# Performance work log

Hardware: AMD Instinct MI355X
Metric: run time of the kernel (lower is better)

Reference implementation:

```python
import jax, jax.numpy as jnp
import numpy as np

B, H, D, DV, N, M = 1, 8, 64, 64, 2048, 128


def setup_inputs() -> dict:
    key = jax.random.key(0)
    k1, k2, k3, k4 = jax.random.split(key, 4)
    keys = jax.random.normal(k1, (B, H, D, N), dtype=jnp.float32)
    values = jax.random.normal(k2, (B, H, DV, N), dtype=jnp.float32)
    queries = jax.random.normal(k3, (B, H, D, N), dtype=jnp.float32)
    # orthonormal random features: QR of (m, key_dim) gaussian (reduced QR, m >= key_dim)
    raw = np.asarray(jax.random.normal(k4, (M, D), dtype=jnp.float32), dtype=np.float64)
    features = jnp.asarray(np.linalg.qr(raw)[0], dtype=jnp.float32)  # (M, D)
    return {"keys": keys, "values": values, "queries": queries, "features": features}


def reference(keys, values, queries, features):
    b, h, d, n = keys.shape
    dv = values.shape[2]
    m = features.shape[0]
    phi_scale = 1.0 / jnp.sqrt(jnp.asarray(m, keys.dtype))
    # flatten heads into batch, move locations to axis 1: (B*H, N, D)
    k = keys.reshape(b * h, d, n).transpose(0, 2, 1)
    v = values.reshape(b * h, dv, n).transpose(0, 2, 1)
    q = queries.reshape(b * h, d, n).transpose(0, 2, 1)

    def phi(x):  # (BH, N, D) -> (BH, N, M); f=[relu], h(x)=1.0
        return jax.nn.relu(jnp.einsum('bnd,md->bnm', x, features)) * phi_scale

    phi_k = phi(k)
    phi_q = phi(q)
    # causal linear attention: prefix sums of phi_k (x) v outer products
    kv = jnp.cumsum(phi_k[:, :, :, None] * v[:, :, None, :], axis=1)  # (BH, N, M, DV)
    out = jnp.einsum('bnm,bnmv->bnv', phi_q, kv)                      # (BH, N, DV)
    norm = jnp.einsum('bnm,bnm->bn', phi_q, jnp.cumsum(phi_k, axis=1))
    out = out / norm[:, :, None]
    out = out.transpose(0, 2, 1).reshape(b, h, dv, n)
    return out
```

## Files before the change

kernel.cpp:

```cpp
#include <hip/hip_runtime.h>


#define BH 8
#define DD 64
#define DV 64
#define NSEQ 2048
#define MM 128
#define CK 32
#define NCH 64
#define NBLK 256
#define PHI_SCALE 0.08838834764831845f

typedef unsigned int uint;
typedef unsigned short ushort;
typedef unsigned long long ulong64;
typedef __attribute__((ext_vector_type(8))) short bf16x8;
typedef __attribute__((ext_vector_type(4))) float f32x4;
#define MFMA16(a, b, c) __builtin_amdgcn_mfma_f32_16x16x32_bf16((a), (b), (c), 0, 0, 0)

__device__ __forceinline__ short f2bf(float x) {
    uint u = __float_as_uint(x);
    u += 0x7fffu + ((u >> 16) & 1u);
    return (short)(u >> 16);
}
__device__ __forceinline__ float bf2f(ushort b) {
    return __uint_as_float(((uint)b) << 16);
}

#define AST(p, v)  __hip_atomic_store((p), (v), __ATOMIC_RELAXED, __HIP_MEMORY_SCOPE_AGENT)
#define ALD(p)     __hip_atomic_load((p), __ATOMIC_RELAXED, __HIP_MEMORY_SCOPE_AGENT)

#define OFF_Z   8388608u
#define OFF_BAR 8650752u

__device__ __forceinline__ void gbar(uint* cnt)
{
    __syncthreads();
    if (threadIdx.x == 0) {
        __hip_atomic_fetch_add(cnt, 1u, __ATOMIC_RELAXED, __HIP_MEMORY_SCOPE_AGENT);
        while (__hip_atomic_load(cnt, __ATOMIC_RELAXED, __HIP_MEMORY_SCOPE_AGENT) < NBLK)
            __builtin_amdgcn_s_sleep(4);
    }
    __syncthreads();
}

__global__ __launch_bounds__(256, 2) void favor_main(
    const float* __restrict__ keys, const float* __restrict__ values,
    const float* __restrict__ queries, const float* __restrict__ features,
    ushort* St, float* z, uint* bar, float* __restrict__ out)
{
    const int b = blockIdx.x;
    const int bh = b >> 5, pr_ = b & 31;
    const int tid = threadIdx.x;
    const int lane = tid & 63, wid = tid >> 6, quad = lane >> 4, l16 = lane & 15;
    const int ch = wid >> 1, sw = wid & 1;
    const int ck = 2 * pr_ + ch, n0c = ck * CK;

    __shared__ __align__(16) char sm[60672];
    short* sPQT = (short*)sm;
    short* sPKT = (short*)(sm + 17408);
    short* sPK  = (short*)(sm + 34816);
    short* sAm  = (short*)(sm + 55296);
    float* sNI  = (float*)(sm + 60416);
    float* sOut = (float*)(sm + 17408);
    float* sPart= (float*)(sm + 34816);
    float* sNm  = (float*)(sm + 36352);
    float* sZ   = (float*)(sm + 36608);

    short* pqt = sPQT + ch * 4352;
    short* pkt = sPKT + ch * 4352;
    short* ppk = sPK + ch * 5120;

    for (int i = tid; i < 1280; i += 256) ((uint*)sAm)[i] = 0u;

    {
        const float* Qb = queries + (size_t)(bh * DD) * NSEQ + n0c + 16 * sw + l16;
        const float* Kb = keys    + (size_t)(bh * DD) * NSEQ + n0c + 16 * sw + l16;
        bf16x8 aQ[2], aK[2];
        for (int h = 0; h < 2; ++h)
            for (int j = 0; j < 8; ++j) {
                const int d = 32 * h + 8 * quad + j;
                aQ[h][j] = f2bf(Qb[(size_t)d * NSEQ]);
                aK[h][j] = f2bf(Kb[(size_t)d * NSEQ]);
            }
        for (int mt = 0; mt < 8; ++mt) {
            f32x4 accQ = {0.f, 0.f, 0.f, 0.f}, accK = {0.f, 0.f, 0.f, 0.f};
            for (int h = 0; h < 2; ++h) {
                const float4* fp = (const float4*)(features + (16 * mt + l16) * 64 + 32 * h + 8 * quad);
                float4 f0 = fp[0], f1 = fp[1];
                bf16x8 bF;
                bF[0] = f2bf(f0.x); bF[1] = f2bf(f0.y); bF[2] = f2bf(f0.z); bF[3] = f2bf(f0.w);
                bF[4] = f2bf(f1.x); bF[5] = f2bf(f1.y); bF[6] = f2bf(f1.z); bF[7] = f2bf(f1.w);
                accQ = MFMA16(aQ[h], bF, accQ);
                accK = MFMA16(aK[h], bF, accK);
            }
            for (int r = 0; r < 4; ++r) {
                const int nl = 16 * sw + 4 * quad + r, m = 16 * mt + l16;
                pqt[nl * 136 + m] = f2bf(fmaxf(accQ[r], 0.f) * PHI_SCALE);
                const short pk = f2bf(fmaxf(accK[r], 0.f) * PHI_SCALE);
                pkt[nl * 136 + m] = pk;
                ppk[m * 40 + nl] = pk;
            }
        }
    }
    __syncthreads();

    {
        const int zch = tid >> 7, m = tid & 127;
        const short* pp = sPK + zch * 5120 + m * 40;
        float s = 0.f;
        for (int n = 0; n < CK; ++n) s += bf2f((ushort)pp[(n + m) & 31]);
        AST(&z[(size_t)(bh * NCH + 2 * pr_ + zch) * MM + m], s);
    }

    {
        ushort* So = St + (size_t)(bh * NCH + ck) * (DV * MM);
        const float* Vb = values + (size_t)(bh * DV) * NSEQ + n0c;
        for (int t = 0; t < 2; ++t) {
            const int vt = 2 * sw + t;
            const float4* vp = (const float4*)(Vb + (size_t)(16 * vt + l16) * NSEQ + 8 * quad);
            float4 v0 = vp[0], v1 = vp[1];
            bf16x8 aV;
            aV[0] = f2bf(v0.x); aV[1] = f2bf(v0.y); aV[2] = f2bf(v0.z); aV[3] = f2bf(v0.w);
            aV[4] = f2bf(v1.x); aV[5] = f2bf(v1.y); aV[6] = f2bf(v1.z); aV[7] = f2bf(v1.w);
            for (int mt = 0; mt < 8; ++mt) {
                bf16x8 bP = *(const bf16x8*)(ppk + (16 * mt + l16) * 40 + 8 * quad);
                f32x4 acc = {0.f, 0.f, 0.f, 0.f};
                acc = MFMA16(aV, bP, acc);
                for (int r = 0; r < 4; ++r)
                    AST(&So[(16 * vt + 4 * quad + r) * MM + 16 * mt + l16],
                        (ushort)f2bf(acc[r]));
            }
        }
    }

    {
        float rs[4] = {0.f, 0.f, 0.f, 0.f};
        for (int jt = 0; jt <= sw; ++jt) {
            f32x4 acc = {0.f, 0.f, 0.f, 0.f};
            for (int mc = 0; mc < 4; ++mc) {
                bf16x8 aP = *(const bf16x8*)(pqt + (16 * sw + l16) * 136 + 32 * mc + 8 * quad);
                bf16x8 bP = *(const bf16x8*)(pkt + (16 * jt + l16) * 136 + 32 * mc + 8 * quad);
                acc = MFMA16(aP, bP, acc);
            }
            for (int r = 0; r < 4; ++r) {
                const int nl = 16 * sw + 4 * quad + r, jl = 16 * jt + l16;
                const float av = (jl <= nl) ? acc[r] : 0.f;
                rs[r] += av;
                sAm[ch * 1280 + nl * 40 + jl] = f2bf(av);
            }
        }
        for (int r = 0; r < 4; ++r) {
            float s = rs[r];
            s += __shfl_xor(s, 1); s += __shfl_xor(s, 2);
            s += __shfl_xor(s, 4); s += __shfl_xor(s, 8);
            if (l16 == 0) sNI[ch * 32 + 16 * sw + 4 * quad + r] = s;
        }
    }

    f32x4 acc[4];
    {
        bf16x8 aA = *(const bf16x8*)(sAm + ch * 1280 + (16 * sw + l16) * 40 + 8 * quad);
        const float* Vb = values + (size_t)(bh * DV) * NSEQ + n0c;
        for (int vt = 0; vt < 4; ++vt) {
            const float4* vp = (const float4*)(Vb + (size_t)(16 * vt + l16) * NSEQ + 8 * quad);
            float4 v0 = vp[0], v1 = vp[1];
            bf16x8 bV;
            bV[0] = f2bf(v0.x); bV[1] = f2bf(v0.y); bV[2] = f2bf(v0.z); bV[3] = f2bf(v0.w);
            bV[4] = f2bf(v1.x); bV[5] = f2bf(v1.y); bV[6] = f2bf(v1.z); bV[7] = f2bf(v1.w);
            acc[vt] = (f32x4){0.f, 0.f, 0.f, 0.f};
            acc[vt] = MFMA16(aA, bV, acc[vt]);
        }
    }

    gbar(bar + 0);
    if (b < 128) {
        const int gid = b * 256 + tid;
        const int sbh = gid >> 12, col = gid & 4095;
        uint* p = (uint*)St + (size_t)sbh * (NCH * 4096) + col;
        float rlo = 0.f, rhi = 0.f;
        for (int half = 0; half < 2; ++half) {
            uint v[32];
            #pragma unroll
            for (int cc = 0; cc < 32; ++cc)
                v[cc] = ALD(p + (size_t)(32 * half + cc) * 4096);
            #pragma unroll
            for (int cc = 0; cc < 32; ++cc) {
                const uint ov = (uint)(ushort)f2bf(rlo) | ((uint)(ushort)f2bf(rhi) << 16);
                AST(p + (size_t)(32 * half + cc) * 4096, ov);
                rlo += bf2f((ushort)(v[cc] & 0xffffu));
                rhi += bf2f((ushort)(v[cc] >> 16));
            }
        }
    } else if (b < 132) {
        const int zc = (b - 128) * 256 + tid;
        const int zbh = zc >> 7, m = zc & 127;
        float* pz = z + (size_t)zbh * (NCH * MM) + m;
        float zr = 0.f;
        for (int half = 0; half < 2; ++half) {
            float zv[32];
            #pragma unroll
            for (int cc = 0; cc < 32; ++cc) zv[cc] = ALD(pz + (32 * half + cc) * MM);
            #pragma unroll
            for (int cc = 0; cc < 32; ++cc) {
                AST(pz + (32 * half + cc) * MM, zr);
                zr += zv[cc];
            }
        }
    }
    gbar(bar + 1);

    {
        const int zch = tid >> 7, m = tid & 127;
        sZ[zch * 128 + m] = ALD(&z[(size_t)(bh * NCH + 2 * pr_ + zch) * MM + m]);
    }
    {
        const ulong64* sb8 = (const ulong64*)(St + (size_t)(bh * NCH + ck) * 8192);
        bf16x8 aP[4];
        for (int mc = 0; mc < 4; ++mc)
            aP[mc] = *(const bf16x8*)(pqt + (16 * sw + l16) * 136 + 32 * mc + 8 * quad);
        for (int vt = 0; vt < 4; ++vt) {
            const int row = 16 * vt + l16;
            for (int mc = 0; mc < 4; ++mc) {
                union { ulong64 u[2]; bf16x8 v; } cvt;
                cvt.u[0] = ALD(sb8 + row * 32 + 8 * mc + 2 * quad);
                cvt.u[1] = ALD(sb8 + row * 32 + 8 * mc + 2 * quad + 1);
                acc[vt] = MFMA16(aP[mc], cvt.v, acc[vt]);
            }
        }
    }
    __syncthreads();
    {
        const int nch = tid >> 7, t2 = tid & 127, n = t2 >> 2, seg = t2 & 3;
        const uint* pr2 = (const uint*)(sPQT + nch * 4352) + n * 68 + seg * 16;
        const float* zz = sZ + nch * 128 + seg * 32;
        float s = 0.f;
        #pragma unroll
        for (int k = 0; k < 16; ++k) {
            const uint u = pr2[k];
            s += bf2f((ushort)(u & 0xffffu)) * zz[2 * k];
            s += bf2f((ushort)(u >> 16)) * zz[2 * k + 1];
        }
        sPart[nch * 128 + n * 4 + seg] = s;
    }
    __syncthreads();
    if (tid < 64) {
        const int nch = tid >> 5, n = tid & 31;
        float nm = sNI[nch * 32 + n];
        #pragma unroll
        for (int s4 = 0; s4 < 4; ++s4) nm += sPart[nch * 128 + n * 4 + s4];
        sNm[nch * 32 + n] = nm;
    }
    __syncthreads();
    for (int vt = 0; vt < 4; ++vt)
        for (int r = 0; r < 4; ++r) {
            const int nl = 16 * sw + 4 * quad + r, v = 16 * vt + l16;
            sOut[ch * 2112 + nl * 66 + v] = acc[vt][r] / sNm[ch * 32 + nl];
        }
    __syncthreads();
    for (int i = tid; i < 4096; i += 256) {
        const int och = i >> 11, rem = i & 2047, v = rem >> 5, n = rem & 31;
        out[(size_t)(bh * DV + v) * NSEQ + (2 * pr_ + och) * CK + n] =
            sOut[och * 2112 + n * 66 + v];
    }
}

extern "C" void kernel_launch(void* const* d_in, const int* in_sizes, int n_in,
                              void* d_out, int out_size, void* d_ws, size_t ws_size,
                              hipStream_t stream)
{
    (void)in_sizes; (void)n_in; (void)out_size; (void)ws_size;
    const float* keys     = (const float*)d_in[0];
    const float* values   = (const float*)d_in[1];
    const float* queries  = (const float*)d_in[2];
    const float* features = (const float*)d_in[3];
    float* outp = (float*)d_out;

    char* ws = (char*)d_ws;
    ushort* St  = (ushort*)ws;
    float*  z   = (float*)(ws + OFF_Z);
    uint*   bar = (uint*)(ws + OFF_BAR);

    hipMemsetAsync(bar, 0, 8, stream);
    favor_main<<<dim3(NBLK), dim3(256), 0, stream>>>(keys, values, queries,
                                                     features, St, z, bar, outp);
}
```

Measured before the change: 104.1 us.

## Split work to one chunk per block, doubling grid to 512 blocks

```diff
diff --git a/kernel.cpp b/kernel.cpp
--- a/kernel.cpp
+++ b/kernel.cpp
@@ -8,7 +8,7 @@
 #define MM 128
 #define CK 32
 #define NCH 64
-#define NBLK 256
+#define NBLK 512
 #define PHI_SCALE 0.08838834764831845f
 
 typedef unsigned int uint;
@@ -50,30 +50,26 @@
     ushort* St, float* z, uint* bar, float* __restrict__ out)
 {
     const int b = blockIdx.x;
-    const int bh = b >> 5, pr_ = b & 31;
+    const int bh = b >> 6, ck = b & 63, n0c = ck * CK;
     const int tid = threadIdx.x;
     const int lane = tid & 63, wid = tid >> 6, quad = lane >> 4, l16 = lane & 15;
-    const int ch = wid >> 1, sw = wid & 1;
-    const int ck = 2 * pr_ + ch, n0c = ck * CK;
-
-    __shared__ __align__(16) char sm[60672];
+
+    __shared__ __align__(16) char sm[30464];
     short* sPQT = (short*)sm;
-    short* sPKT = (short*)(sm + 17408);
-    short* sPK  = (short*)(sm + 34816);
-    short* sAm  = (short*)(sm + 55296);
-    float* sNI  = (float*)(sm + 60416);
-    float* sOut = (float*)(sm + 17408);
-    float* sPart= (float*)(sm + 34816);
-    float* sNm  = (float*)(sm + 36352);
-    float* sZ   = (float*)(sm + 36608);
-
-    short* pqt = sPQT + ch * 4352;
-    short* pkt = sPKT + ch * 4352;
-    short* ppk = sPK + ch * 5120;
-
-    for (int i = tid; i < 1280; i += 256) ((uint*)sAm)[i] = 0u;
-
-    {
+    short* sPKT = (short*)(sm + 8704);
+    short* sPK  = (short*)(sm + 17408);
+    short* sAm  = (short*)(sm + 27648);
+    float* sNI  = (float*)(sm + 30208);
+    float* sOut = (float*)(sm + 8704);
+    float* sPart= (float*)(sm + 17408);
+    float* sNm  = (float*)(sm + 17920);
+    float* sZ   = (float*)(sm + 18048);
+
+    for (int i = tid; i < 640; i += 256) ((uint*)sAm)[i] = 0u;
+    if (tid < 64) sNI[tid] = 0.f;
+
+    {
+        const int sw = wid & 1, mh = wid >> 1;
         const float* Qb = queries + (size_t)(bh * DD) * NSEQ + n0c + 16 * sw + l16;
         const float* Kb = keys    + (size_t)(bh * DD) * NSEQ + n0c + 16 * sw + l16;
         bf16x8 aQ[2], aK[2];
@@ -83,7 +79,8 @@
                 aQ[h][j] = f2bf(Qb[(size_t)d * NSEQ]);
                 aK[h][j] = f2bf(Kb[(size_t)d * NSEQ]);
             }
-        for (int mt = 0; mt < 8; ++mt) {
+        for (int t = 0; t < 4; ++t) {
+            const int mt = 4 * mh + t;
             f32x4 accQ = {0.f, 0.f, 0.f, 0.f}, accK = {0.f, 0.f, 0.f, 0.f};
             for (int h = 0; h < 2; ++h) {
                 const float4* fp = (const float4*)(features + (16 * mt + l16) * 64 + 32 * h + 8 * quad);
@@ -96,80 +93,79 @@
             }
             for (int r = 0; r < 4; ++r) {
                 const int nl = 16 * sw + 4 * quad + r, m = 16 * mt + l16;
-                pqt[nl * 136 + m] = f2bf(fmaxf(accQ[r], 0.f) * PHI_SCALE);
+                sPQT[nl * 136 + m] = f2bf(fmaxf(accQ[r], 0.f) * PHI_SCALE);
                 const short pk = f2bf(fmaxf(accK[r], 0.f) * PHI_SCALE);
-                pkt[nl * 136 + m] = pk;
-                ppk[m * 40 + nl] = pk;
-            }
-        }
-    }
-    __syncthreads();
-
-    {
-        const int zch = tid >> 7, m = tid & 127;
-        const short* pp = sPK + zch * 5120 + m * 40;
+                sPKT[nl * 136 + m] = pk;
+                sPK[m * 40 + nl] = pk;
+            }
+        }
+    }
+    __syncthreads();
+
+    if (tid < 128) {
+        const short* pp = sPK + tid * 40;
         float s = 0.f;
-        for (int n = 0; n < CK; ++n) s += bf2f((ushort)pp[(n + m) & 31]);
-        AST(&z[(size_t)(bh * NCH + 2 * pr_ + zch) * MM + m], s);
-    }
-
-    {
+        for (int n = 0; n < CK; ++n) s += bf2f((ushort)pp[(n + tid) & 31]);
+        AST(&z[(size_t)(bh * NCH + ck) * MM + tid], s);
+    }
+
+    {
+        const int vt = wid;
         ushort* So = St + (size_t)(bh * NCH + ck) * (DV * MM);
-        const float* Vb = values + (size_t)(bh * DV) * NSEQ + n0c;
-        for (int t = 0; t < 2; ++t) {
-            const int vt = 2 * sw + t;
-            const float4* vp = (const float4*)(Vb + (size_t)(16 * vt + l16) * NSEQ + 8 * quad);
-            float4 v0 = vp[0], v1 = vp[1];
-            bf16x8 aV;
-            aV[0] = f2bf(v0.x); aV[1] = f2bf(v0.y); aV[2] = f2bf(v0.z); aV[3] = f2bf(v0.w);
-            aV[4] = f2bf(v1.x); aV[5] = f2bf(v1.y); aV[6] = f2bf(v1.z); aV[7] = f2bf(v1.w);
-            for (int mt = 0; mt < 8; ++mt) {
-                bf16x8 bP = *(const bf16x8*)(ppk + (16 * mt + l16) * 40 + 8 * quad);
-                f32x4 acc = {0.f, 0.f, 0.f, 0.f};
-                acc = MFMA16(aV, bP, acc);
-                for (int r = 0; r < 4; ++r)
-                    AST(&So[(16 * vt + 4 * quad + r) * MM + 16 * mt + l16],
-                        (ushort)f2bf(acc[r]));
-            }
-        }
-    }
-
-    {
-        float rs[4] = {0.f, 0.f, 0.f, 0.f};
-        for (int jt = 0; jt <= sw; ++jt) {
+        const float4* vp = (const float4*)(values + (size_t)(bh * DV + 16 * vt + l16) * NSEQ
+                                           + n0c + 8 * quad);
+        float4 v0 = vp[0], v1 = vp[1];
+        bf16x8 aV;
+        aV[0] = f2bf(v0.x); aV[1] = f2bf(v0.y); aV[2] = f2bf(v0.z); aV[3] = f2bf(v0.w);
+        aV[4] = f2bf(v1.x); aV[5] = f2bf(v1.y); aV[6] = f2bf(v1.z); aV[7] = f2bf(v1.w);
+        for (int mt = 0; mt < 8; ++mt) {
+            bf16x8 bP = *(const bf16x8*)(sPK + (16 * mt + l16) * 40 + 8 * quad);
             f32x4 acc = {0.f, 0.f, 0.f, 0.f};
-            for (int mc = 0; mc < 4; ++mc) {
-                bf16x8 aP = *(const bf16x8*)(pqt + (16 * sw + l16) * 136 + 32 * mc + 8 * quad);
-                bf16x8 bP = *(const bf16x8*)(pkt + (16 * jt + l16) * 136 + 32 * mc + 8 * quad);
-                acc = MFMA16(aP, bP, acc);
-            }
-            for (int r = 0; r < 4; ++r) {
-                const int nl = 16 * sw + 4 * quad + r, jl = 16 * jt + l16;
-                const float av = (jl <= nl) ? acc[r] : 0.f;
-                rs[r] += av;
-                sAm[ch * 1280 + nl * 40 + jl] = f2bf(av);
-            }
+            acc = MFMA16(aV, bP, acc);
+            for (int r = 0; r < 4; ++r)
+                AST(&So[(16 * vt + 4 * quad + r) * MM + 16 * mt + l16],
+                    (ushort)f2bf(acc[r]));
+        }
+    }
+
+    if (wid < 3) {
+        const int swA = (wid >= 1) ? 1 : 0, jtA = (wid == 2) ? 1 : 0;
+        f32x4 acc = {0.f, 0.f, 0.f, 0.f};
+        for (int mc = 0; mc < 4; ++mc) {
+            bf16x8 aP = *(const bf16x8*)(sPQT + (16 * swA + l16) * 136 + 32 * mc + 8 * quad);
+            bf16x8 bP = *(const bf16x8*)(sPKT + (16 * jtA + l16) * 136 + 32 * mc + 8 * quad);
+            acc = MFMA16(aP, bP, acc);
+        }
+        float rs[4];
+        for (int r = 0; r < 4; ++r) {
+            const int nl = 16 * swA + 4 * quad + r, jl = 16 * jtA + l16;
+            const float av = (jl <= nl) ? acc[r] : 0.f;
+            rs[r] = av;
+            sAm[nl * 40 + jl] = f2bf(av);
         }
         for (int r = 0; r < 4; ++r) {
             float s = rs[r];
             s += __shfl_xor(s, 1); s += __shfl_xor(s, 2);
             s += __shfl_xor(s, 4); s += __shfl_xor(s, 8);
-            if (l16 == 0) sNI[ch * 32 + 16 * sw + 4 * quad + r] = s;
-        }
-    }
-
-    f32x4 acc[4];
-    {
-        bf16x8 aA = *(const bf16x8*)(sAm + ch * 1280 + (16 * sw + l16) * 40 + 8 * quad);
-        const float* Vb = values + (size_t)(bh * DV) * NSEQ + n0c;
-        for (int vt = 0; vt < 4; ++vt) {
-            const float4* vp = (const float4*)(Vb + (size_t)(16 * vt + l16) * NSEQ + 8 * quad);
-            float4 v0 = vp[0], v1 = vp[1];
+            if (l16 == 0) sNI[((wid == 2) ? 32 : 0) + 16 * swA + 4 * quad + r] = s;
+        }
+    }
+    __syncthreads();
+
+    const int nt = wid & 1, vp2 = wid >> 1;
+    f32x4 acc[2];
+    {
+        bf16x8 aA = *(const bf16x8*)(sAm + (16 * nt + l16) * 40 + 8 * quad);
+        for (int t = 0; t < 2; ++t) {
+            const int vt = 2 * vp2 + t;
+            const float4* vv = (const float4*)(values + (size_t)(bh * DV + 16 * vt + l16) * NSEQ
+                                               + n0c + 8 * quad);
+            float4 v0 = vv[0], v1 = vv[1];
             bf16x8 bV;
             bV[0] = f2bf(v0.x); bV[1] = f2bf(v0.y); bV[2] = f2bf(v0.z); bV[3] = f2bf(v0.w);
             bV[4] = f2bf(v1.x); bV[5] = f2bf(v1.y); bV[6] = f2bf(v1.z); bV[7] = f2bf(v1.w);
-            acc[vt] = (f32x4){0.f, 0.f, 0.f, 0.f};
-            acc[vt] = MFMA16(aA, bV, acc[vt]);
+            acc[t] = (f32x4){0.f, 0.f, 0.f, 0.f};
+            acc[t] = MFMA16(aA, bV, acc[t]);
         }
     }
 
@@ -178,62 +174,54 @@
         const int gid = b * 256 + tid;
         const int sbh = gid >> 12, col = gid & 4095;
         uint* p = (uint*)St + (size_t)sbh * (NCH * 4096) + col;
+        uint v[NCH];
+        #pragma unroll
+        for (int cc = 0; cc < NCH; ++cc) v[cc] = ALD(p + (size_t)cc * 4096);
         float rlo = 0.f, rhi = 0.f;
-        for (int half = 0; half < 2; ++half) {
-            uint v[32];
-            #pragma unroll
-            for (int cc = 0; cc < 32; ++cc)
-                v[cc] = ALD(p + (size_t)(32 * half + cc) * 4096);
-            #pragma unroll
-            for (int cc = 0; cc < 32; ++cc) {
-                const uint ov = (uint)(ushort)f2bf(rlo) | ((uint)(ushort)f2bf(rhi) << 16);
-                AST(p + (size_t)(32 * half + cc) * 4096, ov);
-                rlo += bf2f((ushort)(v[cc] & 0xffffu));
-                rhi += bf2f((ushort)(v[cc] >> 16));
-            }
+        #pragma unroll
+        for (int cc = 0; cc < NCH; ++cc) {
+            const uint ov = (uint)(ushort)f2bf(rlo) | ((uint)(ushort)f2bf(rhi) << 16);
+            AST(p + (size_t)cc * 4096, ov);
+            rlo += bf2f((ushort)(v[cc] & 0xffffu));
+            rhi += bf2f((ushort)(v[cc] >> 16));
         }
     } else if (b < 132) {
         const int zc = (b - 128) * 256 + tid;
         const int zbh = zc >> 7, m = zc & 127;
         float* pz = z + (size_t)zbh * (NCH * MM) + m;
+        float zv[NCH];
+        #pragma unroll
+        for (int cc = 0; cc < NCH; ++cc) zv[cc] = ALD(pz + cc * MM);
         float zr = 0.f;
-        for (int half = 0; half < 2; ++half) {
-            float zv[32];
-            #pragma unroll
-            for (int cc = 0; cc < 32; ++cc) zv[cc] = ALD(pz + (32 * half + cc) * MM);
-            #pragma unroll
-            for (int cc = 0; cc < 32; ++cc) {
-                AST(pz + (32 * half + cc) * MM, zr);
-                zr += zv[cc];
-            }
+        #pragma unroll
+        for (int cc = 0; cc < NCH; ++cc) {
+            AST(pz + cc * MM, zr);
+            zr += zv[cc];
         }
     }
     gbar(bar + 1);
 
-    {
-        const int zch = tid >> 7, m = tid & 127;
-        sZ[zch * 128 + m] = ALD(&z[(size_t)(bh * NCH + 2 * pr_ + zch) * MM + m]);
-    }
+    if (tid < 128) sZ[tid] = ALD(&z[(size_t)(bh * NCH + ck) * MM + tid]);
     {
         const ulong64* sb8 = (const ulong64*)(St + (size_t)(bh * NCH + ck) * 8192);
         bf16x8 aP[4];
         for (int mc = 0; mc < 4; ++mc)
-            aP[mc] = *(const bf16x8*)(pqt + (16 * sw + l16) * 136 + 32 * mc + 8 * quad);
-        for (int vt = 0; vt < 4; ++vt) {
-            const int row = 16 * vt + l16;
+            aP[mc] = *(const bf16x8*)(sPQT + (16 * nt + l16) * 136 + 32 * mc + 8 * quad);
+        for (int t = 0; t < 2; ++t) {
+            const int row = 16 * (2 * vp2 + t) + l16;
             for (int mc = 0; mc < 4; ++mc) {
                 union { ulong64 u[2]; bf16x8 v; } cvt;
                 cvt.u[0] = ALD(sb8 + row * 32 + 8 * mc + 2 * quad);
                 cvt.u[1] = ALD(sb8 + row * 32 + 8 * mc + 2 * quad + 1);
-                acc[vt] = MFMA16(aP[mc], cvt.v, acc[vt]);
-            }
-        }
-    }
-    __syncthreads();
-    {
-        const int nch = tid >> 7, t2 = tid & 127, n = t2 >> 2, seg = t2 & 3;
-        const uint* pr2 = (const uint*)(sPQT + nch * 4352) + n * 68 + seg * 16;
-        const float* zz = sZ + nch * 128 + seg * 32;
+                acc[t] = MFMA16(aP[mc], cvt.v, acc[t]);
+            }
+        }
+    }
+    __syncthreads();
+    if (tid < 128) {
+        const int n = tid >> 2, seg = tid & 3;
+        const uint* pr2 = (const uint*)sPQT + n * 68 + seg * 16;
+        const float* zz = sZ + seg * 32;
         float s = 0.f;
         #pragma unroll
         for (int k = 0; k < 16; ++k) {
@@ -241,27 +229,25 @@
             s += bf2f((ushort)(u & 0xffffu)) * zz[2 * k];
             s += bf2f((ushort)(u >> 16)) * zz[2 * k + 1];
         }
-        sPart[nch * 128 + n * 4 + seg] = s;
-    }
-    __syncthreads();
-    if (tid < 64) {
-        const int nch = tid >> 5, n = tid & 31;
-        float nm = sNI[nch * 32 + n];
-        #pragma unroll
-        for (int s4 = 0; s4 < 4; ++s4) nm += sPart[nch * 128 + n * 4 + s4];
-        sNm[nch * 32 + n] = nm;
-    }
-    __syncthreads();
-    for (int vt = 0; vt < 4; ++vt)
+        sPart[n * 4 + seg] = s;
+    }
+    __syncthreads();
+    if (tid < 32) {
+        float nm = sNI[tid] + sNI[32 + tid];
+        #pragma unroll
+        for (int s4 = 0; s4 < 4; ++s4) nm += sPart[tid * 4 + s4];
+        sNm[tid] = nm;
+    }
+    __syncthreads();
+    for (int t = 0; t < 2; ++t)
         for (int r = 0; r < 4; ++r) {
-            const int nl = 16 * sw + 4 * quad + r, v = 16 * vt + l16;
-            sOut[ch * 2112 + nl * 66 + v] = acc[vt][r] / sNm[ch * 32 + nl];
-        }
-    __syncthreads();
-    for (int i = tid; i < 4096; i += 256) {
-        const int och = i >> 11, rem = i & 2047, v = rem >> 5, n = rem & 31;
-        out[(size_t)(bh * DV + v) * NSEQ + (2 * pr_ + och) * CK + n] =
-            sOut[och * 2112 + n * 66 + v];
+            const int nl = 16 * nt + 4 * quad + r, v = 16 * (2 * vp2 + t) + l16;
+            sOut[nl * 66 + v] = acc[t][r] / sNm[nl];
+        }
+    __syncthreads();
+    for (int i = tid; i < 2048; i += 256) {
+        const int v = i >> 5, n = i & 31;
+        out[(size_t)(bh * DV + v) * NSEQ + n0c + n] = sOut[n * 66 + v];
     }
 }
 
```

Result: slower. 112.6 us (+8.2%).
